# Optimization experiments

Hardware: AMD Instinct MI355X
Metric: run time of the kernel (lower is better)

The kernel has to match this reference:

```python
import jax, jax.numpy as jnp
import numpy as np
from jax import lax

N_BITS = 16


def ripple_add(a_bin, b_bin):
    """Bit-serial ripple-carry add. a_bin, b_bin: (N, n_bits) int32 in {0,1}.
    Returns (sum_bits, carry_bits), each (N, n_bits) int32."""
    def step(c, ab):
        ai, bi = ab
        s = ai ^ bi ^ c
        cn = (ai & bi) | (ai & c) | (bi & c)
        return cn, (s, cn)

    c0 = jnp.zeros(a_bin.shape[0], jnp.int32)
    _, (s, c) = lax.scan(step, c0, (a_bin.T, b_bin.T))
    return s.T, c.T


def setup_inputs() -> dict:
    key = jax.random.key(0)
    k1, k2 = jax.random.split(key)
    B, K, nb = 65536, 4, N_BITS
    x = jax.random.randint(k1, (B, K, nb), 0, 2).astype(jnp.float32)
    p = jax.random.uniform(k2, (B * K, nb), dtype=jnp.float32)
    return {"x": x, "p": p}


def reference(x, p):
    B, K, nb = x.shape
    # residual computed under no_grad in the original
    powers_f = 2.0 ** jnp.arange(nb, dtype=jnp.float32)
    x_sum = (x.sum(axis=-2) * powers_f).sum(axis=-1)            # (B,)
    x_int = (x * powers_f).sum(axis=-1)                          # (B, K)
    resid_int = (x_sum[:, None] - x_int).astype(jnp.int32)       # (B, K)
    powers_i = (2 ** jnp.arange(nb)).astype(jnp.int32)
    x_residual = ((resid_int[..., None] & powers_i) > 0).astype(jnp.float32)  # (B, K, nb)

    a_bin = jnp.round(x.reshape(-1, nb)).astype(jnp.int32)
    b_bin = jnp.round(x_residual.reshape(-1, nb)).astype(jnp.int32)
    s, c = ripple_add(a_bin, b_bin)

    out = s.astype(jnp.float32).reshape(B, K, nb).mean(axis=-2)    # (B, nb)
    carry = c.astype(jnp.float32).reshape(B, K, nb).sum(axis=-2)   # (B, nb)
    return out, carry
```

## Files before the change

### kernel.cpp

```cpp
#include <hip/hip_runtime.h>

__global__ __launch_bounds__(256) void sga_kernel(const float* __restrict__ x,
                                                  float* __restrict__ out,
                                                  int BK) {
    int t = blockIdx.x * blockDim.x + threadIdx.x;
    if (t >= BK) return;

    const float4* xp = reinterpret_cast<const float4*>(x) + (size_t)t * 4;
    float4 v0 = xp[0], v1 = xp[1], v2 = xp[2], v3 = xp[3];

    unsigned a = 0;
    a |= (unsigned)(v0.x != 0.0f) << 0;
    a |= (unsigned)(v0.y != 0.0f) << 1;
    a |= (unsigned)(v0.z != 0.0f) << 2;
    a |= (unsigned)(v0.w != 0.0f) << 3;
    a |= (unsigned)(v1.x != 0.0f) << 4;
    a |= (unsigned)(v1.y != 0.0f) << 5;
    a |= (unsigned)(v1.z != 0.0f) << 6;
    a |= (unsigned)(v1.w != 0.0f) << 7;
    a |= (unsigned)(v2.x != 0.0f) << 8;
    a |= (unsigned)(v2.y != 0.0f) << 9;
    a |= (unsigned)(v2.z != 0.0f) << 10;
    a |= (unsigned)(v2.w != 0.0f) << 11;
    a |= (unsigned)(v3.x != 0.0f) << 12;
    a |= (unsigned)(v3.y != 0.0f) << 13;
    a |= (unsigned)(v3.z != 0.0f) << 14;
    a |= (unsigned)(v3.w != 0.0f) << 15;

    unsigned tot = a + __shfl_xor(a, 1);
    tot += __shfl_xor(tot, 2);
    unsigned bb = (tot - a) & 0xFFFFu;

    unsigned sum = a + bb;
    unsigned s   = sum & 0xFFFFu;
    unsigned cin = a ^ bb ^ s;
    unsigned c   = (cin >> 1) | (((sum >> 16) & 1u) << 15);

    auto spread8 = [](unsigned b) {
        unsigned u = (b | (b << 12)) & 0x000F000Fu;
        u = (u | (u << 6)) & 0x03030303u;
        u = (u | (u << 3)) & 0x11111111u;
        return u;
    };
    unsigned long long ss = (unsigned long long)spread8(s & 0xFFu) |
                            ((unsigned long long)spread8((s >> 8) & 0xFFu) << 32);
    unsigned long long cc = (unsigned long long)spread8(c & 0xFFu) |
                            ((unsigned long long)spread8((c >> 8) & 0xFFu) << 32);

    ss += __shfl_xor(ss, 1); ss += __shfl_xor(ss, 2);
    cc += __shfl_xor(cc, 1); cc += __shfl_xor(cc, 2);

    int sh = (t & 3) * 16;
    float4 o, ca;
    o.x  = (float)((ss >> (sh + 0))  & 0xFULL) * 0.25f;
    o.y  = (float)((ss >> (sh + 4))  & 0xFULL) * 0.25f;
    o.z  = (float)((ss >> (sh + 8))  & 0xFULL) * 0.25f;
    o.w  = (float)((ss >> (sh + 12)) & 0xFULL) * 0.25f;
    ca.x = (float)((cc >> (sh + 0))  & 0xFULL);
    ca.y = (float)((cc >> (sh + 4))  & 0xFULL);
    ca.z = (float)((cc >> (sh + 8))  & 0xFULL);
    ca.w = (float)((cc >> (sh + 12)) & 0xFULL);

    float4* outv = reinterpret_cast<float4*>(out);
    outv[t]      = o;
    outv[BK + t] = ca;
}

extern "C" void kernel_launch(void* const* d_in, const int* in_sizes, int n_in,
                              void* d_out, int out_size, void* d_ws, size_t ws_size,
                              hipStream_t stream) {
    const float* x = (const float*)d_in[0];
    float* out = (float*)d_out;
    int BK = in_sizes[0] / 16;
    int threads = 256;
    int blocks = (BK + threads - 1) / threads;
    sga_kernel<<<blocks, threads, 0, stream>>>(x, out, BK);
}
```

Baseline: 10.44 us.

## Process whole row per thread with bitsliced counting instead of lane shuffles

```diff
diff --git a/kernel.cpp b/kernel.cpp
--- a/kernel.cpp
+++ b/kernel.cpp
@@ -1,78 +1,83 @@
 #include <hip/hip_runtime.h>
 
-__global__ __launch_bounds__(256) void sga_kernel(const float* __restrict__ x,
-                                                  float* __restrict__ out,
-                                                  int BK) {
-    int t = blockIdx.x * blockDim.x + threadIdx.x;
-    if (t >= BK) return;
+__global__ __launch_bounds__(256) void sga_row_kernel(const uint4* __restrict__ x,
+                                                      float* __restrict__ out,
+                                                      int B) {
+    int b = blockIdx.x * blockDim.x + threadIdx.x;
+    if (b >= B) return;
 
-    const float4* xp = reinterpret_cast<const float4*>(x) + (size_t)t * 4;
-    float4 v0 = xp[0], v1 = xp[1], v2 = xp[2], v3 = xp[3];
+    const uint4* xp = x + (size_t)b * 16;
 
-    unsigned a = 0;
-    a |= (unsigned)(v0.x != 0.0f) << 0;
-    a |= (unsigned)(v0.y != 0.0f) << 1;
-    a |= (unsigned)(v0.z != 0.0f) << 2;
-    a |= (unsigned)(v0.w != 0.0f) << 3;
-    a |= (unsigned)(v1.x != 0.0f) << 4;
-    a |= (unsigned)(v1.y != 0.0f) << 5;
-    a |= (unsigned)(v1.z != 0.0f) << 6;
-    a |= (unsigned)(v1.w != 0.0f) << 7;
-    a |= (unsigned)(v2.x != 0.0f) << 8;
-    a |= (unsigned)(v2.y != 0.0f) << 9;
-    a |= (unsigned)(v2.z != 0.0f) << 10;
-    a |= (unsigned)(v2.w != 0.0f) << 11;
-    a |= (unsigned)(v3.x != 0.0f) << 12;
-    a |= (unsigned)(v3.y != 0.0f) << 13;
-    a |= (unsigned)(v3.z != 0.0f) << 14;
-    a |= (unsigned)(v3.w != 0.0f) << 15;
+    unsigned a0 = 0, a1 = 0, a2 = 0, a3 = 0;
+    #pragma unroll
+    for (int q = 0; q < 4; ++q) {
+        uint4 v0 = xp[0 * 4 + q];
+        uint4 v1 = xp[1 * 4 + q];
+        uint4 v2 = xp[2 * 4 + q];
+        uint4 v3 = xp[3 * 4 + q];
+        int sh = q * 4;
+        a0 |= (((v0.x >> 23) & 1u) << (sh + 0)) | (((v0.y >> 23) & 1u) << (sh + 1)) |
+              (((v0.z >> 23) & 1u) << (sh + 2)) | (((v0.w >> 23) & 1u) << (sh + 3));
+        a1 |= (((v1.x >> 23) & 1u) << (sh + 0)) | (((v1.y >> 23) & 1u) << (sh + 1)) |
+              (((v1.z >> 23) & 1u) << (sh + 2)) | (((v1.w >> 23) & 1u) << (sh + 3));
+        a2 |= (((v2.x >> 23) & 1u) << (sh + 0)) | (((v2.y >> 23) & 1u) << (sh + 1)) |
+              (((v2.z >> 23) & 1u) << (sh + 2)) | (((v2.w >> 23) & 1u) << (sh + 3));
+        a3 |= (((v3.x >> 23) & 1u) << (sh + 0)) | (((v3.y >> 23) & 1u) << (sh + 1)) |
+              (((v3.z >> 23) & 1u) << (sh + 2)) | (((v3.w >> 23) & 1u) << (sh + 3));
+    }
 
-    unsigned tot = a + __shfl_xor(a, 1);
-    tot += __shfl_xor(tot, 2);
-    unsigned bb = (tot - a) & 0xFFFFu;
+    unsigned tot = a0 + a1 + a2 + a3;
 
-    unsigned sum = a + bb;
-    unsigned s   = sum & 0xFFFFu;
-    unsigned cin = a ^ bb ^ s;
-    unsigned c   = (cin >> 1) | (((sum >> 16) & 1u) << 15);
+    unsigned s[4], c[4], a[4] = {a0, a1, a2, a3};
+    #pragma unroll
+    for (int k = 0; k < 4; ++k) {
+        unsigned bb  = (tot - a[k]) & 0xFFFFu;
+        unsigned sum = a[k] + bb;
+        unsigned sk  = sum & 0xFFFFu;
+        unsigned cin = a[k] ^ bb ^ sk;
+        s[k] = sk;
+        c[k] = (cin >> 1) | (((sum >> 16) & 1u) << 15);
+    }
 
-    auto spread8 = [](unsigned b) {
-        unsigned u = (b | (b << 12)) & 0x000F000Fu;
-        u = (u | (u << 6)) & 0x03030303u;
-        u = (u | (u << 3)) & 0x11111111u;
-        return u;
+    auto vcount = [](const unsigned* v, unsigned& p0, unsigned& p1, unsigned& p2) {
+        unsigned l01 = v[0] ^ v[1], h01 = v[0] & v[1];
+        unsigned l23 = v[2] ^ v[3], h23 = v[2] & v[3];
+        p0 = l01 ^ l23;
+        unsigned cr = l01 & l23;
+        p1 = h01 ^ h23 ^ cr;
+        p2 = (h01 & h23) | (h01 & cr) | (h23 & cr);
     };
-    unsigned long long ss = (unsigned long long)spread8(s & 0xFFu) |
-                            ((unsigned long long)spread8((s >> 8) & 0xFFu) << 32);
-    unsigned long long cc = (unsigned long long)spread8(c & 0xFFu) |
-                            ((unsigned long long)spread8((c >> 8) & 0xFFu) << 32);
+    unsigned sp0, sp1, sp2, cp0, cp1, cp2;
+    vcount(s, sp0, sp1, sp2);
+    vcount(c, cp0, cp1, cp2);
 
-    ss += __shfl_xor(ss, 1); ss += __shfl_xor(ss, 2);
-    cc += __shfl_xor(cc, 1); cc += __shfl_xor(cc, 2);
+    float4* ov = reinterpret_cast<float4*>(out) + (size_t)b * 4;
+    float4* cv = reinterpret_cast<float4*>(out) + ((size_t)B + b) * 4;
 
-    int sh = (t & 3) * 16;
-    float4 o, ca;
-    o.x  = (float)((ss >> (sh + 0))  & 0xFULL) * 0.25f;
-    o.y  = (float)((ss >> (sh + 4))  & 0xFULL) * 0.25f;
-    o.z  = (float)((ss >> (sh + 8))  & 0xFULL) * 0.25f;
-    o.w  = (float)((ss >> (sh + 12)) & 0xFULL) * 0.25f;
-    ca.x = (float)((cc >> (sh + 0))  & 0xFULL);
-    ca.y = (float)((cc >> (sh + 4))  & 0xFULL);
-    ca.z = (float)((cc >> (sh + 8))  & 0xFULL);
-    ca.w = (float)((cc >> (sh + 12)) & 0xFULL);
-
-    float4* outv = reinterpret_cast<float4*>(out);
-    outv[t]      = o;
-    outv[BK + t] = ca;
+    #pragma unroll
+    for (int q = 0; q < 4; ++q) {
+        int i0 = q * 4;
+        float4 o, ca;
+        o.x = (float)(((sp0 >> (i0 + 0)) & 1u) | ((((sp1 >> (i0 + 0)) & 1u) << 1)) | ((((sp2 >> (i0 + 0)) & 1u) << 2))) * 0.25f;
+        o.y = (float)(((sp0 >> (i0 + 1)) & 1u) | ((((sp1 >> (i0 + 1)) & 1u) << 1)) | ((((sp2 >> (i0 + 1)) & 1u) << 2))) * 0.25f;
+        o.z = (float)(((sp0 >> (i0 + 2)) & 1u) | ((((sp1 >> (i0 + 2)) & 1u) << 1)) | ((((sp2 >> (i0 + 2)) & 1u) << 2))) * 0.25f;
+        o.w = (float)(((sp0 >> (i0 + 3)) & 1u) | ((((sp1 >> (i0 + 3)) & 1u) << 1)) | ((((sp2 >> (i0 + 3)) & 1u) << 2))) * 0.25f;
+        ca.x = (float)(((cp0 >> (i0 + 0)) & 1u) | ((((cp1 >> (i0 + 0)) & 1u) << 1)) | ((((cp2 >> (i0 + 0)) & 1u) << 2)));
+        ca.y = (float)(((cp0 >> (i0 + 1)) & 1u) | ((((cp1 >> (i0 + 1)) & 1u) << 1)) | ((((cp2 >> (i0 + 1)) & 1u) << 2)));
+        ca.z = (float)(((cp0 >> (i0 + 2)) & 1u) | ((((cp1 >> (i0 + 2)) & 1u) << 1)) | ((((cp2 >> (i0 + 2)) & 1u) << 2)));
+        ca.w = (float)(((cp0 >> (i0 + 3)) & 1u) | ((((cp1 >> (i0 + 3)) & 1u) << 1)) | ((((cp2 >> (i0 + 3)) & 1u) << 2)));
+        ov[q] = o;
+        cv[q] = ca;
+    }
 }
 
 extern "C" void kernel_launch(void* const* d_in, const int* in_sizes, int n_in,
                               void* d_out, int out_size, void* d_ws, size_t ws_size,
                               hipStream_t stream) {
-    const float* x = (const float*)d_in[0];
+    const uint4* x = (const uint4*)d_in[0];
     float* out = (float*)d_out;
-    int BK = in_sizes[0] / 16;
+    int B = in_sizes[0] / 64;
     int threads = 256;
-    int blocks = (BK + threads - 1) / threads;
-    sga_kernel<<<blocks, threads, 0, stream>>>(x, out, BK);
+    int blocks = (B + threads - 1) / threads;
+    sga_row_kernel<<<blocks, threads, 0, stream>>>(x, out, B);
 }
```

Result: slower. 11.95 us (+14.4%).
